# Performance work log

Hardware: AMD Instinct MI355X
Metric: run time of the kernel (lower is better)

## Reference

```python
import jax, jax.numpy as jnp
import numpy as np

DIM, SEQ, HEADS, HDIM, BATCH, VOCAB, NVOCAB = 512, 1024, 8, 64, 8, 1024, 3
EPS = 1e-5


def layer_norm(x, g, b):
    mu = x.mean(-1, keepdims=True)
    var = x.var(-1, keepdims=True)
    return (x - mu) * jax.lax.rsqrt(var + EPS) * g + b


def multiscale_retention(x, Wq, Wk, Wv, Wg, Wo):
    B, S, D = x.shape
    def split(h):  # [B,S,D] -> [B,H,S,hd]
        return h.reshape(B, S, HEADS, HDIM).transpose(0, 2, 1, 3)
    q, k, v = split(x @ Wq), split(x @ Wk), split(x @ Wv)
    # RetNet per-head decays and causal decay matrix D[h,n,m] = gamma_h^(n-m), n>=m
    gammas = 1.0 - 2.0 ** (-5.0 - jnp.arange(HEADS, dtype=jnp.float32))
    n = jnp.arange(S)
    diff = n[:, None] - n[None, :]
    decay = jnp.where(diff >= 0, gammas[:, None, None] ** jnp.maximum(diff, 0).astype(jnp.float32), 0.0)
    scores = jnp.einsum('bhsd,bhtd->bhst', q, k) * (1.0 / np.sqrt(HDIM))
    y = jnp.einsum('bhst,bhtd->bhsd', scores * decay, v)
    # group norm per head (no affine)
    mu = y.mean(-1, keepdims=True)
    var = y.var(-1, keepdims=True)
    y = (y - mu) * jax.lax.rsqrt(var + EPS)
    y = y.transpose(0, 2, 1, 3).reshape(B, S, D)
    gate = jax.nn.swish(x @ Wg)
    return (gate * y) @ Wo


def feed_forward(x, W1, b1, W2, b2):
    return jax.nn.relu(x @ W1 + b1) @ W2 + b2


def setup_inputs() -> dict:
    key = jax.random.key(0)
    ks = jax.random.split(key, 12)
    s = 0.02
    return {
        'ids': jax.random.randint(ks[0], (NVOCAB, BATCH, SEQ), 0, VOCAB),
        'emb_tables': jax.random.normal(ks[1], (NVOCAB, VOCAB, DIM), jnp.float32) * s,
        'pos_emb': jax.random.normal(ks[2], (NVOCAB, SEQ, DIM), jnp.float32) * s,
        'ln_gamma': jnp.ones((DIM,), jnp.float32),
        'ln_beta': jnp.zeros((DIM,), jnp.float32),
        'Wq': jax.random.normal(ks[3], (DIM, DIM), jnp.float32) * s,
        'Wk': jax.random.normal(ks[4], (DIM, DIM), jnp.float32) * s,
        'Wv': jax.random.normal(ks[5], (DIM, DIM), jnp.float32) * s,
        'Wg': jax.random.normal(ks[6], (DIM, DIM), jnp.float32) * s,
        'Wo': jax.random.normal(ks[7], (DIM, DIM), jnp.float32) * s,
        'W1': jax.random.normal(ks[8], (DIM, DIM), jnp.float32) * s,
        'b1': jnp.zeros((DIM,), jnp.float32),
        'W2': jax.random.normal(ks[9], (DIM, DIM), jnp.float32) * s,
        'b2': jnp.zeros((DIM,), jnp.float32),
        'fc_W': jax.random.normal(ks[10], (SEQ * DIM, 1), jnp.float32) * s,
        'fc_b': jnp.zeros((1,), jnp.float32),
    }


def reference(ids, emb_tables, pos_emb, ln_gamma, ln_beta, Wq, Wk, Wv, Wg, Wo,
              W1, b1, W2, b2, fc_W, fc_b):
    x = None
    for i in range(NVOCAB):  # loop over vocab embeddings, x overwritten each pass (as in source)
        emb = emb_tables[i][ids[i]] + pos_emb[i][None, :, :]  # [B,S,D]
        x = layer_norm(emb, ln_gamma, ln_beta)
        x = multiscale_retention(x, Wq, Wk, Wv, Wg, Wo) + x
        x = feed_forward(layer_norm(x, ln_gamma, ln_beta), W1, b1, W2, b2) + x
        x = layer_norm(x, ln_gamma, ln_beta)
    flat = x.reshape(x.shape[0], -1)  # Flatten
    return jax.nn.sigmoid(flat @ fc_W + fc_b)  # dropout inactive at inference
```

## Files before the change

kernel.cpp:

```cpp
#include <hip/hip_runtime.h>
#include <math.h>

typedef unsigned short u16;
typedef __attribute__((ext_vector_type(8))) _Float16 half8;
typedef __attribute__((ext_vector_type(4))) float f32x4;
typedef __attribute__((ext_vector_type(4))) unsigned short us4;


static __device__ __forceinline__ u16 f2h(float f) {
    _Float16 h = (_Float16)f;
    return __builtin_bit_cast(u16, h);
}
static __device__ __forceinline__ float h2f(u16 u) {
    return (float)__builtin_bit_cast(_Float16, u);
}
static __device__ __forceinline__ void gl_lds16(const void* g, void* l) {
    __builtin_amdgcn_global_load_lds(
        (const __attribute__((address_space(1))) void*)g,
        (__attribute__((address_space(3))) void*)l, 16, 0, 0);
}

__global__ __launch_bounds__(256) void prep_kernel(
    const float* __restrict__ Wq, const float* __restrict__ Wk, const float* __restrict__ Wv,
    const float* __restrict__ Wg, const float* __restrict__ Wo, const float* __restrict__ W1,
    const float* __restrict__ W2, u16* __restrict__ WT,
    const int* __restrict__ ids, const float* __restrict__ emb, const float* __restrict__ pos,
    const float* __restrict__ gam, const float* __restrict__ bet, u16* __restrict__ x0h)
{
    __shared__ float tile[64][65];
    int bx = blockIdx.x, t = threadIdx.x;
    if (bx < 448) {
        const float* Ws[7] = {Wq, Wk, Wv, Wg, Wo, W1, W2};
        int w = bx >> 6, rem = bx & 63;
        int k0 = (rem >> 3) * 64, n0 = (rem & 7) * 64;
        const float* W = Ws[w];
        for (int c = t; c < 4096; c += 256) {
            int row = c >> 6, col = c & 63;
            tile[row][col] = W[(size_t)(k0 + row) * 512 + n0 + col];
        }
        __syncthreads();
        for (int c = t; c < 4096; c += 256) {
            int row = c >> 6, col = c & 63;
            WT[(size_t)w * 262144 + (size_t)(n0 + row) * 512 + k0 + col] = f2h(tile[col][row]);
        }
    } else {
        int wid = t >> 6, lane = t & 63;
        int row = (bx - 448) * 4 + wid;
        int col = lane * 8;
        int id = ids[2 * 8192 + row];
        const float* e = emb + (size_t)(2 * 1024 + id) * 512 + col;
        const float* p = pos + (size_t)(2 * 1024 + (row & 1023)) * 512 + col;
        float4 e0 = *(const float4*)e, e1 = *(const float4*)(e + 4);
        float4 p0 = *(const float4*)p, p1 = *(const float4*)(p + 4);
        float v[8] = {e0.x + p0.x, e0.y + p0.y, e0.z + p0.z, e0.w + p0.w,
                      e1.x + p1.x, e1.y + p1.y, e1.z + p1.z, e1.w + p1.w};
        float s1 = 0.f, s2 = 0.f;
#pragma unroll
        for (int j = 0; j < 8; ++j) { s1 += v[j]; s2 += v[j] * v[j]; }
#pragma unroll
        for (int o = 32; o >= 1; o >>= 1) {
            s1 += __shfl_xor(s1, o, 64);
            s2 += __shfl_xor(s2, o, 64);
        }
        float mu = s1 * (1.f / 512.f);
        float var = fmaxf(s2 * (1.f / 512.f) - mu * mu, 0.f);
        float rs = 1.f / sqrtf(var + 1e-5f);
        float4 g0 = *(const float4*)&gam[col], g1 = *(const float4*)&gam[col + 4];
        float4 b0 = *(const float4*)&bet[col], b1 = *(const float4*)&bet[col + 4];
        float gv[8] = {g0.x, g0.y, g0.z, g0.w, g1.x, g1.y, g1.z, g1.w};
        float bv[8] = {b0.x, b0.y, b0.z, b0.w, b1.x, b1.y, b1.z, b1.w};
        half8 hv;
#pragma unroll
        for (int j = 0; j < 8; ++j) hv[j] = (_Float16)((v[j] - mu) * rs * gv[j] + bv[j]);
        *(half8*)&x0h[(size_t)row * 512 + col] = hv;
    }
}

__global__ __launch_bounds__(256) void ln_kernel(
    const u16* __restrict__ xin,
    const float* __restrict__ gam, const float* __restrict__ bet,
    u16* __restrict__ outh,
    const float* __restrict__ fcW, float* __restrict__ fcpart)
{
    int wid = threadIdx.x >> 6, lane = threadIdx.x & 63;
    int row = blockIdx.x * 4 + wid;
    int col = lane * 8;
    float v[8];
    half8 x = *(const half8*)&xin[(size_t)row * 512 + col];
#pragma unroll
    for (int j = 0; j < 8; ++j) v[j] = (float)x[j];
    float s1 = 0.f, s2 = 0.f;
#pragma unroll
    for (int j = 0; j < 8; ++j) { s1 += v[j]; s2 += v[j] * v[j]; }
#pragma unroll
    for (int o = 32; o >= 1; o >>= 1) {
        s1 += __shfl_xor(s1, o, 64);
        s2 += __shfl_xor(s2, o, 64);
    }
    float mu = s1 * (1.f / 512.f);
    float var = fmaxf(s2 * (1.f / 512.f) - mu * mu, 0.f);
    float rs = 1.f / sqrtf(var + 1e-5f);
    float4 g0 = *(const float4*)&gam[col], g1 = *(const float4*)&gam[col + 4];
    float4 b0 = *(const float4*)&bet[col], b1 = *(const float4*)&bet[col + 4];
    float gv[8] = {g0.x, g0.y, g0.z, g0.w, g1.x, g1.y, g1.z, g1.w};
    float bv[8] = {b0.x, b0.y, b0.z, b0.w, b1.x, b1.y, b1.z, b1.w};
    float y[8];
#pragma unroll
    for (int j = 0; j < 8; ++j) y[j] = (v[j] - mu) * rs * gv[j] + bv[j];
    if (outh) {
        half8 hv;
#pragma unroll
        for (int j = 0; j < 8; ++j) hv[j] = (_Float16)y[j];
        *(half8*)&outh[(size_t)row * 512 + col] = hv;
    }
    if (fcW) {
        int srow = row & 1023;
        const float* wp = &fcW[(size_t)srow * 512 + col];
        float4 w0 = *(const float4*)wp, w1 = *(const float4*)(wp + 4);
        float d = y[0] * w0.x + y[1] * w0.y + y[2] * w0.z + y[3] * w0.w +
                  y[4] * w1.x + y[5] * w1.y + y[6] * w1.z + y[7] * w1.w;
#pragma unroll
        for (int o = 32; o >= 1; o >>= 1) d += __shfl_xor(d, o, 64);
        if (lane == 0) fcpart[row] = d;
    }
}

__global__ __launch_bounds__(256) void gemm_f16(
    const u16* __restrict__ A2, const u16* __restrict__ Bg,
    u16* __restrict__ outh, int ostride)
{
    __shared__ u16 As[128 * 64];
    __shared__ u16 Bs[128 * 64];
    int t = threadIdx.x;
    int wid = t >> 6, lane = t & 63, quad = lane >> 4, l15 = lane & 15;
    int wm = wid >> 1, wn = wid & 1;
    int orig = blockIdx.x;
    int wgid = (orig & 7) * 128 + (orig >> 3);
    int m0 = (wgid >> 4) * 128, n0 = (wgid & 15) * 128;

    int srow = wid * 8 + (lane >> 3);
    int scol = (lane & 7) * 8;

    f32x4 acc[4][4];
#pragma unroll
    for (int a = 0; a < 4; ++a)
#pragma unroll
        for (int b = 0; b < 4; ++b) acc[a][b] = (f32x4){0.f, 0.f, 0.f, 0.f};

    for (int ki = 0; ki < 8; ++ki) {
        int k0 = ki * 64;
        __syncthreads();
#pragma unroll
        for (int i = 0; i < 4; ++i) {
            int r = i * 32 + srow;
            gl_lds16(&A2[(size_t)(m0 + r) * 512 + k0 + scol], &As[(i * 32 + wid * 8) * 64]);
            gl_lds16(&Bg[(size_t)(n0 + r) * 512 + k0 + scol], &Bs[(i * 32 + wid * 8) * 64]);
        }
        __syncthreads();
#pragma unroll
        for (int ks = 0; ks < 2; ++ks) {
            half8 af[4], bf[4];
#pragma unroll
            for (int tm = 0; tm < 4; ++tm)
                af[tm] = *(const half8*)&As[(wm * 64 + tm * 16 + l15) * 64 + ks * 32 + quad * 8];
#pragma unroll
            for (int tn = 0; tn < 4; ++tn)
                bf[tn] = *(const half8*)&Bs[(wn * 64 + tn * 16 + l15) * 64 + ks * 32 + quad * 8];
#pragma unroll
            for (int tm = 0; tm < 4; ++tm)
#pragma unroll
                for (int tn = 0; tn < 4; ++tn)
                    acc[tm][tn] = __builtin_amdgcn_mfma_f32_16x16x32_f16(af[tm], bf[tn], acc[tm][tn], 0, 0, 0);
        }
    }

#pragma unroll
    for (int hb = 0; hb < 2; ++hb) {
        __syncthreads();
        if (wm == hb) {
#pragma unroll
            for (int tm = 0; tm < 4; ++tm)
#pragma unroll
                for (int tn = 0; tn < 4; ++tn)
#pragma unroll
                    for (int r = 0; r < 4; ++r) {
                        int rl = tm * 16 + quad * 4 + r;
                        int cl = wn * 64 + tn * 16 + l15;
                        As[rl * 128 + cl] = f2h(acc[tm][tn][r]);
                    }
        }
        __syncthreads();
#pragma unroll
        for (int i = 0; i < 4; ++i) {
            int c = t + i * 256;
            int row = c >> 4, ch = c & 15;
            *(half8*)&outh[(size_t)(m0 + hb * 64 + row) * ostride + n0 + ch * 8] =
                *(const half8*)&As[row * 128 + ch * 8];
        }
    }
}

__global__ __launch_bounds__(256) void gemm_f16_n64(
    const u16* __restrict__ A2, const u16* __restrict__ Bg,
    u16* __restrict__ outh,
    const u16* __restrict__ res, const float* __restrict__ bias, int mode)
{
    __shared__ u16 As[128 * 64];
    __shared__ u16 Bs[64 * 64];
    int t = threadIdx.x;
    int wid = t >> 6, lane = t & 63, quad = lane >> 4, l15 = lane & 15;
    int orig = blockIdx.x;
    int wgid = (orig & 7) * 64 + (orig >> 3);
    int m0 = (wgid >> 3) * 128, n0 = (wgid & 7) * 64;

    int srow = wid * 8 + (lane >> 3);
    int scol = (lane & 7) * 8;

    f32x4 acc[2][4];
#pragma unroll
    for (int a = 0; a < 2; ++a)
#pragma unroll
        for (int b = 0; b < 4; ++b) acc[a][b] = (f32x4){0.f, 0.f, 0.f, 0.f};

    for (int ki = 0; ki < 8; ++ki) {
        int k0 = ki * 64;
        __syncthreads();
#pragma unroll
        for (int i = 0; i < 4; ++i) {
            int r = i * 32 + srow;
            gl_lds16(&A2[(size_t)(m0 + r) * 512 + k0 + scol], &As[(i * 32 + wid * 8) * 64]);
        }
#pragma unroll
        for (int i = 0; i < 2; ++i) {
            int r = i * 32 + srow;
            gl_lds16(&Bg[(size_t)(n0 + r) * 512 + k0 + scol], &Bs[(i * 32 + wid * 8) * 64]);
        }
        __syncthreads();
#pragma unroll
        for (int ks = 0; ks < 2; ++ks) {
            half8 af[2], bf[4];
#pragma unroll
            for (int tm = 0; tm < 2; ++tm)
                af[tm] = *(const half8*)&As[(wid * 32 + tm * 16 + l15) * 64 + ks * 32 + quad * 8];
#pragma unroll
            for (int tn = 0; tn < 4; ++tn)
                bf[tn] = *(const half8*)&Bs[(tn * 16 + l15) * 64 + ks * 32 + quad * 8];
#pragma unroll
            for (int tm = 0; tm < 2; ++tm)
#pragma unroll
                for (int tn = 0; tn < 4; ++tn)
                    acc[tm][tn] = __builtin_amdgcn_mfma_f32_16x16x32_f16(af[tm], bf[tn], acc[tm][tn], 0, 0, 0);
        }
    }

    __syncthreads();
#pragma unroll
    for (int tm = 0; tm < 2; ++tm) {
#pragma unroll
        for (int tn = 0; tn < 4; ++tn) {
            int n = n0 + tn * 16 + l15;
#pragma unroll
            for (int r = 0; r < 4; ++r) {
                int rl = wid * 32 + tm * 16 + quad * 4 + r;
                int m = m0 + rl;
                float v = acc[tm][tn][r];
                if (mode == 1) v += h2f(res[(size_t)m * 512 + n]);
                else if (mode == 2) v = fmaxf(v + bias[n], 0.f);
                else if (mode == 3) v += bias[n] + h2f(res[(size_t)m * 512 + n]);
                As[rl * 64 + tn * 16 + l15] = f2h(v);
            }
        }
    }
    __syncthreads();
#pragma unroll
    for (int i = 0; i < 4; ++i) {
        int c = t + i * 256;
        int row = c >> 3, ch = c & 7;
        *(half8*)&outh[(size_t)(m0 + row) * 512 + n0 + ch * 8] =
            *(const half8*)&As[row * 64 + ch * 8];
    }
}

__global__ __launch_bounds__(256) void chunk_t(
    const u16* __restrict__ QKVGh, u16* __restrict__ Tst)
{
    __shared__ u16 kth[64 * 144];
    __shared__ u16 vth[64 * 144];
    int t = threadIdx.x;
    int wid = t >> 6, lane = t & 63, quad = lane >> 4, l15 = lane & 15;
    int bh = blockIdx.x >> 3, c = blockIdx.x & 7;
    int b = bh >> 3, h = bh & 7;
    float gamma = 1.f - exp2f(-(float)(5 + h));
    float l2g = log2f(gamma);

    for (int cc = t; cc < 2048; cc += 256) {
        int d = cc & 63, mseg = cc >> 6;
        size_t gbase = (size_t)(b * 1024 + c * 128 + mseg * 4) * 2048 + h * 64 + d;
        us4 k4, v4;
#pragma unroll
        for (int i = 0; i < 4; ++i) {
            float kv = h2f(QKVGh[gbase + 512 + (size_t)i * 2048]);
            k4[i] = f2h(kv * exp2f((float)(127 - (mseg * 4 + i)) * l2g));
            v4[i] = QKVGh[gbase + 1024 + (size_t)i * 2048];
        }
        int base = d * 144 + (((mseg >> 1) + d) & 15) * 8 + (mseg & 1) * 4;
        *(us4*)&kth[base] = k4;
        *(us4*)&vth[base] = v4;
    }
    __syncthreads();
    f32x4 T[4];
#pragma unroll
    for (int dt = 0; dt < 4; ++dt) T[dt] = (f32x4){0.f, 0.f, 0.f, 0.f};
    int ra = wid * 16 + l15;
#pragma unroll
    for (int ks = 0; ks < 4; ++ks) {
        half8 av = *(const half8*)&vth[ra * 144 + ((ks * 4 + quad + ra) & 15) * 8];
#pragma unroll
        for (int dt = 0; dt < 4; ++dt) {
            int rb = dt * 16 + l15;
            half8 bk = *(const half8*)&kth[rb * 144 + ((ks * 4 + quad + rb) & 15) * 8];
            T[dt] = __builtin_amdgcn_mfma_f32_16x16x32_f16(av, bk, T[dt], 0, 0, 0);
        }
    }
#pragma unroll
    for (int dt = 0; dt < 4; ++dt)
#pragma unroll
        for (int r = 0; r < 4; ++r) {
            int i = wid * 16 + quad * 4 + r;
            int j = dt * 16 + l15;
            Tst[(((size_t)bh * 8 + c) * 64 + i) * 64 + j] = f2h(T[dt][r]);
        }
}

__global__ __launch_bounds__(256) void retention_f16(
    const u16* __restrict__ QKVGh, const u16* __restrict__ Tst, u16* __restrict__ Zh)
{
    __shared__ u16 kh[128 * 64];
    __shared__ u16 vth[64 * 144];
    __shared__ u16 ph[4][16 * 132];

    int t = threadIdx.x;
    int wid = t >> 6, lane = t & 63, quad = lane >> 4, l15 = lane & 15;
    int bh = blockIdx.x >> 3, qt = blockIdx.x & 7;
    int b = bh >> 3, h = bh & 7;
    int n0 = qt * 128;

    float gamma = 1.f - exp2f(-(float)(5 + h));
    float l2g = log2f(gamma);

    {
        int srow = wid * 8 + (lane >> 3);
        int scol = (lane & 7) * 8;
#pragma unroll
        for (int i = 0; i < 4; ++i) {
            int r = i * 32 + srow;
            gl_lds16(&QKVGh[(size_t)(b * 1024 + n0 + r) * 2048 + 512 + h * 64 + scol],
                     &kh[(i * 32 + wid * 8) * 64]);
        }
    }
    for (int c = t; c < 2048; c += 256) {
        int d = c & 63, mseg = c >> 6;
        size_t gbase = (size_t)(b * 1024 + n0 + mseg * 4) * 2048 + 1024 + h * 64 + d;
        us4 v4 = {QKVGh[gbase], QKVGh[gbase + 2048],
                  QKVGh[gbase + 4096], QKVGh[gbase + 6144]};
        int base = d * 144 + (((mseg >> 1) + d) & 15) * 8 + (mseg & 1) * 4;
        *(us4*)&vth[base] = v4;
    }

    half8 aH[2][2], aHs[2][2];
#pragma unroll
    for (int g = 0; g < 2; ++g) {
        int rowloc = wid * 32 + g * 16 + l15;
        int qrow = b * 1024 + n0 + rowloc;
        const u16* qp = QKVGh + (size_t)qrow * 2048 + h * 64;
        float qs = exp2f((float)(rowloc + 1) * l2g - 3.f);
#pragma unroll
        for (int ks = 0; ks < 2; ++ks) {
            aH[g][ks] = *(const half8*)&qp[ks * 32 + quad * 8];
#pragma unroll
            for (int j = 0; j < 8; ++j)
                aHs[g][ks][j] = (_Float16)((float)aH[g][ks][j] * qs);
        }
    }

    half8 sf[2][4];
    if (qt > 0) {
        float sa[2][4][8];
#pragma unroll
        for (int ks = 0; ks < 2; ++ks)
#pragma unroll
            for (int dt = 0; dt < 4; ++dt)
#pragma unroll
                for (int j = 0; j < 8; ++j) sa[ks][dt][j] = 0.f;
        for (int c = 0; c < qt; ++c) {
            float sc = exp2f((float)(128 * (qt - 1 - c)) * l2g);
            const u16* tp = &Tst[((size_t)bh * 8 + c) * 4096];
#pragma unroll
            for (int ks = 0; ks < 2; ++ks)
#pragma unroll
                for (int dt = 0; dt < 4; ++dt) {
                    half8 tv = *(const half8*)&tp[(dt * 16 + l15) * 64 + ks * 32 + quad * 8];
#pragma unroll
                    for (int j = 0; j < 8; ++j) sa[ks][dt][j] += sc * (float)tv[j];
                }
        }
#pragma unroll
        for (int ks = 0; ks < 2; ++ks)
#pragma unroll
            for (int dt = 0; dt < 4; ++dt)
#pragma unroll
                for (int j = 0; j < 8; ++j) sf[ks][dt][j] = (_Float16)sa[ks][dt][j];
    }
    __syncthreads();

    f32x4 yacc[2][4];
#pragma unroll
    for (int g = 0; g < 2; ++g)
#pragma unroll
        for (int dt = 0; dt < 4; ++dt) yacc[g][dt] = (f32x4){0.f, 0.f, 0.f, 0.f};

    if (qt > 0) {
#pragma unroll
        for (int ks = 0; ks < 2; ++ks)
#pragma unroll
            for (int g = 0; g < 2; ++g)
#pragma unroll
                for (int dt = 0; dt < 4; ++dt)
                    yacc[g][dt] = __builtin_amdgcn_mfma_f32_16x16x32_f16(aHs[g][ks], sf[ks][dt], yacc[g][dt], 0, 0, 0);
    }

#pragma unroll
    for (int g = 0; g < 2; ++g) {
        f32x4 sacc[8];
#pragma unroll
        for (int tn = 0; tn < 8; ++tn) sacc[tn] = (f32x4){0.f, 0.f, 0.f, 0.f};
#pragma unroll
        for (int tn = 0; tn < 8; ++tn)
#pragma unroll
            for (int ks = 0; ks < 2; ++ks) {
                half8 bH = *(const half8*)&kh[(tn * 16 + l15) * 64 + ks * 32 + quad * 8];
                sacc[tn] = __builtin_amdgcn_mfma_f32_16x16x32_f16(aH[g][ks], bH, sacc[tn], 0, 0, 0);
            }
#pragma unroll
        for (int tn = 0; tn < 8; ++tn) {
            int mloc = tn * 16 + l15;
#pragma unroll
            for (int r = 0; r < 4; ++r) {
                int nloc = wid * 32 + g * 16 + quad * 4 + r;
                int diff = nloc - mloc;
                float p = (diff >= 0) ? sacc[tn][r] * exp2f((float)diff * l2g - 3.0f) : 0.f;
                ph[wid][(quad * 4 + r) * 132 + tn * 16 + l15] = f2h(p);
            }
        }
        half8 pH[4];
#pragma unroll
        for (int ks = 0; ks < 4; ++ks)
            pH[ks] = *(const half8*)&ph[wid][l15 * 132 + ks * 32 + quad * 8];
#pragma unroll
        for (int dt = 0; dt < 4; ++dt) {
            int d = dt * 16 + l15;
#pragma unroll
            for (int ks = 0; ks < 4; ++ks) {
                half8 vv = *(const half8*)&vth[d * 144 + ((ks * 4 + quad + d) & 15) * 8];
                yacc[g][dt] = __builtin_amdgcn_mfma_f32_16x16x32_f16(pH[ks], vv, yacc[g][dt], 0, 0, 0);
            }
        }
    }

#pragma unroll
    for (int g = 0; g < 2; ++g) {
#pragma unroll
        for (int r = 0; r < 4; ++r) {
            float s1 = yacc[g][0][r] + yacc[g][1][r] + yacc[g][2][r] + yacc[g][3][r];
            float s2 = yacc[g][0][r] * yacc[g][0][r] + yacc[g][1][r] * yacc[g][1][r] +
                       yacc[g][2][r] * yacc[g][2][r] + yacc[g][3][r] * yacc[g][3][r];
#pragma unroll
            for (int o = 1; o <= 8; o <<= 1) {
                s1 += __shfl_xor(s1, o, 64);
                s2 += __shfl_xor(s2, o, 64);
            }
            float mu = s1 * (1.f / 64.f);
            float var = fmaxf(s2 * (1.f / 64.f) - mu * mu, 0.f);
            float rs = 1.f / sqrtf(var + 1e-5f);
            int nglob = n0 + wid * 32 + g * 16 + quad * 4 + r;
            size_t grow = (size_t)(b * 1024 + nglob);
#pragma unroll
            for (int dt = 0; dt < 4; ++dt) {
                int d = dt * 16 + l15;
                float yv = (yacc[g][dt][r] - mu) * rs;
                float gt = h2f(QKVGh[grow * 2048 + 1536 + h * 64 + d]);
                float sw = gt / (1.f + expf(-gt));
                Zh[grow * 512 + h * 64 + d] = f2h(yv * sw);
            }
        }
    }
}

__global__ __launch_bounds__(256) void fc_final(const float* __restrict__ fcpart,
                                                const float* __restrict__ fcb,
                                                float* __restrict__ out)
{
    __shared__ float red[4];
    int b = blockIdx.x, t = threadIdx.x;
    float4 v = *(const float4*)&fcpart[(size_t)b * 1024 + t * 4];
    float s = v.x + v.y + v.z + v.w;
    int wid = t >> 6, lane = t & 63;
#pragma unroll
    for (int o = 32; o >= 1; o >>= 1) s += __shfl_xor(s, o, 64);
    if (lane == 0) red[wid] = s;
    __syncthreads();
    if (t == 0) {
        float l = red[0] + red[1] + red[2] + red[3] + fcb[0];
        out[b] = 1.f / (1.f + expf(-l));
    }
}

extern "C" void kernel_launch(void* const* d_in, const int* in_sizes, int n_in,
                              void* d_out, int out_size, void* d_ws, size_t ws_size,
                              hipStream_t stream)
{
    const int* ids = (const int*)d_in[0];
    const float* emb = (const float*)d_in[1];
    const float* pos = (const float*)d_in[2];
    const float* ln_g = (const float*)d_in[3];
    const float* ln_b = (const float*)d_in[4];
    const float* Wq = (const float*)d_in[5];
    const float* Wk = (const float*)d_in[6];
    const float* Wv = (const float*)d_in[7];
    const float* Wg = (const float*)d_in[8];
    const float* Wo = (const float*)d_in[9];
    const float* W1 = (const float*)d_in[10];
    const float* b1 = (const float*)d_in[11];
    const float* W2 = (const float*)d_in[12];
    const float* b2 = (const float*)d_in[13];
    const float* fcW = (const float*)d_in[14];
    const float* fcb = (const float*)d_in[15];
    float* out = (float*)d_out;

    char* ws = (char*)d_ws;
    u16* WT     = (u16*)(ws);
    u16* x0h    = (u16*)(ws + 3670016);
    u16* Zh     = (u16*)(ws + 12058624);
    u16* QKVGh  = (u16*)(ws + 20447232);
    float* fcpart = (float*)(ws + 54001664);
    u16* Tst    = (u16*)(ws + 54034432);
    u16* X1h = QKVGh;
    u16* Th  = (u16*)((char*)QKVGh + 8388608);
    u16* Hh  = (u16*)((char*)QKVGh + 16777216);
    u16* X2h = Zh;

    prep_kernel<<<2496, 256, 0, stream>>>(Wq, Wk, Wv, Wg, Wo, W1, W2, WT,
                                          ids, emb, pos, ln_g, ln_b, x0h);
    gemm_f16<<<1024, 256, 0, stream>>>(x0h, WT, QKVGh, 2048);
    chunk_t<<<512, 256, 0, stream>>>(QKVGh, Tst);
    retention_f16<<<512, 256, 0, stream>>>(QKVGh, Tst, Zh);
    gemm_f16_n64<<<512, 256, 0, stream>>>(Zh, WT + 4 * 262144, X1h, x0h, nullptr, 1);
    ln_kernel<<<2048, 256, 0, stream>>>(X1h, ln_g, ln_b, Th, nullptr, nullptr);
    gemm_f16_n64<<<512, 256, 0, stream>>>(Th, WT + 5 * 262144, Hh, nullptr, b1, 2);
    gemm_f16_n64<<<512, 256, 0, stream>>>(Hh, WT + 6 * 262144, X2h, X1h, b2, 3);
    ln_kernel<<<2048, 256, 0, stream>>>(X2h, ln_g, ln_b, nullptr, fcW, fcpart);
    fc_final<<<8, 256, 0, stream>>>(fcpart, fcb, out);
}
```

Before: 221.9 us.

## Rewrite QKVG GEMM with 256x256 tiles and 4-stage async LDS pipeline

Replaces the 128x128, 256-thread QKVG projection GEMM with a 256x256-tile, 512-thread kernel. It uses a 4-slot ring buffer of async global-to-LDS loads with explicit vmcnt waits and raises wave priority around the MFMA blocks. The aim is to overlap global loads with matrix math and cut per-output load traffic through larger tiles. In exchange it uses 128KB of LDS and twice the accumulator registers, and it launches only 256 blocks, so occupancy and load balance across CUs may suffer.

```diff
diff --git a/kernel.cpp b/kernel.cpp
--- a/kernel.cpp
+++ b/kernel.cpp
@@ -125,78 +125,108 @@
     }
 }
 
-__global__ __launch_bounds__(256) void gemm_f16(
+static __device__ __forceinline__ void stage_tile(
+    const u16* pa0, const u16* pa1, const u16* pb0, const u16* pb1,
+    u16* ldsw, int slot, int kt)
+{
+    int off = kt * 32;
+    u16* d = ldsw + slot * 16384;
+    gl_lds16(pa0 + off, d);
+    gl_lds16(pa1 + off, d + 4096);
+    gl_lds16(pb0 + off, d + 8192);
+    gl_lds16(pb1 + off, d + 12288);
+}
+
+static __device__ __forceinline__ void compute_tile(
+    const u16* lds, int slot, int wm, int wn, int quad, int l15, f32x4 (&acc)[8][4])
+{
+    const u16* A = lds + slot * 16384;
+    const u16* B = A + 8192;
+    __builtin_amdgcn_s_setprio(1);
+#pragma unroll
+    for (int mq = 0; mq < 2; ++mq)
+#pragma unroll
+        for (int nq = 0; nq < 2; ++nq) {
+            half8 a[4], b[2];
+#pragma unroll
+            for (int i = 0; i < 4; ++i)
+                a[i] = *(const half8*)&A[(wm * 128 + mq * 64 + i * 16 + l15) * 32 + quad * 8];
+#pragma unroll
+            for (int j = 0; j < 2; ++j)
+                b[j] = *(const half8*)&B[(wn * 64 + nq * 32 + j * 16 + l15) * 32 + quad * 8];
+#pragma unroll
+            for (int i = 0; i < 4; ++i)
+#pragma unroll
+                for (int j = 0; j < 2; ++j)
+                    acc[mq * 4 + i][nq * 2 + j] = __builtin_amdgcn_mfma_f32_16x16x32_f16(
+                        a[i], b[j], acc[mq * 4 + i][nq * 2 + j], 0, 0, 0);
+        }
+    __builtin_amdgcn_s_setprio(0);
+}
+
+#define QITER(KT, VM)                                                              \
+    do {                                                                           \
+        if ((KT) + 3 < 16) stage_tile(pa0, pa1, pb0, pb1, ldsw, ((KT) + 3) & 3, (KT) + 3); \
+        asm volatile("s_waitcnt vmcnt(" #VM ")" ::: "memory");                     \
+        __builtin_amdgcn_s_barrier();                                              \
+        asm volatile("" ::: "memory");                                             \
+        compute_tile(lds, (KT) & 3, wm, wn, quad, l15, acc);                       \
+        asm volatile("" ::: "memory");                                             \
+        __builtin_amdgcn_s_barrier();                                              \
+    } while (0)
+
+__global__ __launch_bounds__(512, 2) void gemm_f16(
     const u16* __restrict__ A2, const u16* __restrict__ Bg,
     u16* __restrict__ outh, int ostride)
 {
-    __shared__ u16 As[128 * 64];
-    __shared__ u16 Bs[128 * 64];
+    __shared__ u16 lds[65536];
     int t = threadIdx.x;
     int wid = t >> 6, lane = t & 63, quad = lane >> 4, l15 = lane & 15;
-    int wm = wid >> 1, wn = wid & 1;
+    int wm = wid >> 2, wn = wid & 3;
     int orig = blockIdx.x;
-    int wgid = (orig & 7) * 128 + (orig >> 3);
-    int m0 = (wgid >> 4) * 128, n0 = (wgid & 15) * 128;
-
-    int srow = wid * 8 + (lane >> 3);
-    int scol = (lane & 7) * 8;
-
-    f32x4 acc[4][4];
-#pragma unroll
-    for (int a = 0; a < 4; ++a)
-#pragma unroll
-        for (int b = 0; b < 4; ++b) acc[a][b] = (f32x4){0.f, 0.f, 0.f, 0.f};
-
-    for (int ki = 0; ki < 8; ++ki) {
-        int k0 = ki * 64;
-        __syncthreads();
-#pragma unroll
-        for (int i = 0; i < 4; ++i) {
-            int r = i * 32 + srow;
-            gl_lds16(&A2[(size_t)(m0 + r) * 512 + k0 + scol], &As[(i * 32 + wid * 8) * 64]);
-            gl_lds16(&Bg[(size_t)(n0 + r) * 512 + k0 + scol], &Bs[(i * 32 + wid * 8) * 64]);
-        }
-        __syncthreads();
-#pragma unroll
-        for (int ks = 0; ks < 2; ++ks) {
-            half8 af[4], bf[4];
-#pragma unroll
-            for (int tm = 0; tm < 4; ++tm)
-                af[tm] = *(const half8*)&As[(wm * 64 + tm * 16 + l15) * 64 + ks * 32 + quad * 8];
-#pragma unroll
-            for (int tn = 0; tn < 4; ++tn)
-                bf[tn] = *(const half8*)&Bs[(wn * 64 + tn * 16 + l15) * 64 + ks * 32 + quad * 8];
-#pragma unroll
-            for (int tm = 0; tm < 4; ++tm)
-#pragma unroll
-                for (int tn = 0; tn < 4; ++tn)
-                    acc[tm][tn] = __builtin_amdgcn_mfma_f32_16x16x32_f16(af[tm], bf[tn], acc[tm][tn], 0, 0, 0);
-        }
-    }
-
-#pragma unroll
-    for (int hb = 0; hb < 2; ++hb) {
-        __syncthreads();
-        if (wm == hb) {
-#pragma unroll
-            for (int tm = 0; tm < 4; ++tm)
-#pragma unroll
-                for (int tn = 0; tn < 4; ++tn)
-#pragma unroll
-                    for (int r = 0; r < 4; ++r) {
-                        int rl = tm * 16 + quad * 4 + r;
-                        int cl = wn * 64 + tn * 16 + l15;
-                        As[rl * 128 + cl] = f2h(acc[tm][tn][r]);
-                    }
-        }
-        __syncthreads();
-#pragma unroll
-        for (int i = 0; i < 4; ++i) {
-            int c = t + i * 256;
-            int row = c >> 4, ch = c & 15;
-            *(half8*)&outh[(size_t)(m0 + hb * 64 + row) * ostride + n0 + ch * 8] =
-                *(const half8*)&As[row * 128 + ch * 8];
-        }
+    int wgid = (orig & 7) * 32 + (orig >> 3);
+    int m0 = (wgid >> 3) * 256, n0 = (wgid & 7) * 256;
+
+    int srow = t >> 2, sc = (t & 3) * 8;
+    const u16* pa0 = A2 + (size_t)(m0 + srow) * 512 + sc;
+    const u16* pa1 = pa0 + (size_t)128 * 512;
+    const u16* pb0 = Bg + (size_t)(n0 + srow) * 512 + sc;
+    const u16* pb1 = pb0 + (size_t)128 * 512;
+    u16* ldsw = lds + wid * 512;
+
+    f32x4 acc[8][4];
+#pragma unroll
+    for (int i = 0; i < 8; ++i)
+#pragma unroll
+        for (int j = 0; j < 4; ++j) acc[i][j] = (f32x4){0.f, 0.f, 0.f, 0.f};
+
+    stage_tile(pa0, pa1, pb0, pb1, ldsw, 0, 0);
+    stage_tile(pa0, pa1, pb0, pb1, ldsw, 1, 1);
+    stage_tile(pa0, pa1, pb0, pb1, ldsw, 2, 2);
+
+    QITER(0, 12);  QITER(1, 12);  QITER(2, 12);  QITER(3, 12);
+    QITER(4, 12);  QITER(5, 12);  QITER(6, 12);  QITER(7, 12);
+    QITER(8, 12);  QITER(9, 12);  QITER(10, 12); QITER(11, 12);
+    QITER(12, 12);
+    QITER(13, 8);  QITER(14, 4);  QITER(15, 0);
+
+    u16* C = lds;
+#pragma unroll
+    for (int i = 0; i < 8; ++i)
+#pragma unroll
+        for (int j = 0; j < 4; ++j)
+#pragma unroll
+            for (int r = 0; r < 4; ++r)
+                C[(wm * 128 + i * 16 + quad * 4 + r) * 256 + wn * 64 + j * 16 + l15] =
+                    f2h(acc[i][j][r]);
+    __builtin_amdgcn_s_barrier();
+    asm volatile("" ::: "memory");
+#pragma unroll
+    for (int it = 0; it < 16; ++it) {
+        int idx = it * 512 + t;
+        int row = idx >> 5, ch = idx & 31;
+        *(half8*)&outh[(size_t)(m0 + row) * ostride + n0 + ch * 8] =
+            *(const half8*)&C[row * 256 + ch * 8];
     }
 }
 
@@ -551,7 +581,7 @@
 
     prep_kernel<<<2496, 256, 0, stream>>>(Wq, Wk, Wv, Wg, Wo, W1, W2, WT,
                                           ids, emb, pos, ln_g, ln_b, x0h);
-    gemm_f16<<<1024, 256, 0, stream>>>(x0h, WT, QKVGh, 2048);
+    gemm_f16<<<256, 512, 0, stream>>>(x0h, WT, QKVGh, 2048);
     chunk_t<<<512, 256, 0, stream>>>(QKVGh, Tst);
     retention_f16<<<512, 256, 0, stream>>>(QKVGh, Tst, Zh);
     gemm_f16_n64<<<512, 256, 0, stream>>>(Zh, WT + 4 * 262144, X1h, x0h, nullptr, 1);
```

Measured after the change: 213.2 us. 1.04x faster.
